# Optimization experiments

Hardware: AMD Instinct MI355X
Metric: run time of the kernel (lower is better)

Reference implementation:

```python
import jax, jax.numpy as jnp
import numpy as np

N_NODES = 50000
N_HYPEREDGES = 20000


def _segment_softmax(logits, seg, num_segments):
    mx = jax.ops.segment_max(logits, seg, num_segments=num_segments)
    mx = jnp.where(jnp.isfinite(mx), mx, 0.0)
    e = jnp.exp(logits - mx[seg])
    s = jax.ops.segment_sum(e, seg, num_segments=num_segments)
    return e / (s[seg] + 1e-16)


def _hypergraph_conv(x, he_node, he_edge, W, bias, num_nodes, num_he):
    # PyG HypergraphConv (use_attention=False, heads=1, hyperedge_weight=1):
    # out = D^{-1} H B^{-1} H^T (x W) + bias
    h = x @ W  # [N, C]
    ones = jnp.ones_like(he_node, dtype=h.dtype)
    D = jax.ops.segment_sum(ones, he_node, num_segments=num_nodes)
    Dinv = jnp.where(D > 0, 1.0 / D, 0.0)
    B = jax.ops.segment_sum(ones, he_edge, num_segments=num_he)
    Binv = jnp.where(B > 0, 1.0 / B, 0.0)
    # node -> hyperedge
    m = Binv[:, None] * jax.ops.segment_sum(h[he_node], he_edge, num_segments=num_he)
    # hyperedge -> node
    out = Dinv[:, None] * jax.ops.segment_sum(m[he_edge], he_node, num_segments=num_nodes)
    return out + bias


def _gat_conv(x, edge_index, W, a_src, a_dst, bias, num_nodes):
    # PyG GATConv defaults: heads=1, concat=True, slope=0.2, add_self_loops=True
    loops = jnp.arange(num_nodes)
    src = jnp.concatenate([edge_index[0], loops])
    dst = jnp.concatenate([edge_index[1], loops])
    h = x @ W  # [N, C]
    asrc = h @ a_src  # [N]
    adst = h @ a_dst  # [N]
    logit = jax.nn.leaky_relu(asrc[src] + adst[dst], negative_slope=0.2)
    alpha = _segment_softmax(logit, dst, num_nodes)  # softmax over incoming edges
    out = jax.ops.segment_sum(alpha[:, None] * h[src], dst, num_segments=num_nodes)
    return out + bias


def _mlp(e, Wm1, bm1, Wm2, bm2, Wm3, bm3, Wm4, bm4):
    # PyG MLP(128,64,3, num_layers=4) in eval mode: BN is identity at init,
    # dropout inactive -> Linear+ReLU chain, final Linear plain.
    h = jax.nn.relu(e @ Wm1 + bm1)
    h = jax.nn.relu(h @ Wm2 + bm2)
    h = jax.nn.relu(h @ Wm3 + bm3)
    return h @ Wm4 + bm4


def setup_inputs() -> dict:
    key = jax.random.key(0)
    ks = jax.random.split(key, 32)
    s = 0.05
    inp = {
        'x': jax.random.normal(ks[0], (N_NODES, 128), dtype=jnp.float32),
        'edge_index': jax.random.randint(ks[1], (2, 800000), 0, N_NODES),
        'he_node': jax.random.randint(ks[2], (400000,), 0, N_NODES),
        'he_edge': jax.random.randint(ks[3], (400000,), 0, N_HYPEREDGES),
        'edge_label_index': jax.random.randint(ks[4], (2, 100000), 0, N_NODES),
        'W1': jax.random.normal(ks[5], (128, 256)) * s,
        'b1': jnp.zeros((256,), jnp.float32),
        'W2': jax.random.normal(ks[6], (256, 256)) * s,
        'a2s': jax.random.normal(ks[7], (256,)) * s,
        'a2d': jax.random.normal(ks[8], (256,)) * s,
        'b2': jnp.zeros((256,), jnp.float32),
        'W3': jax.random.normal(ks[9], (256, 64)) * s,
        'a3s': jax.random.normal(ks[10], (64,)) * s,
        'a3d': jax.random.normal(ks[11], (64,)) * s,
        'b3': jnp.zeros((64,), jnp.float32),
        'Wm1': jax.random.normal(ks[12], (128, 64)) * s,
        'bm1': jnp.zeros((64,), jnp.float32),
        'Wm2': jax.random.normal(ks[13], (64, 64)) * s,
        'bm2': jnp.zeros((64,), jnp.float32),
        'Wm3': jax.random.normal(ks[14], (64, 64)) * s,
        'bm3': jnp.zeros((64,), jnp.float32),
        'Wm4': jax.random.normal(ks[15], (64, 3)) * s,
        'bm4': jnp.zeros((3,), jnp.float32),
    }
    return inp


def reference(x, edge_index, he_node, he_edge, edge_label_index,
              W1, b1, W2, a2s, a2d, b2, W3, a3s, a3d, b3,
              Wm1, bm1, Wm2, bm2, Wm3, bm3, Wm4, bm4):
    n = x.shape[0]
    # encode
    h = jax.nn.relu(_hypergraph_conv(x, he_node, he_edge, W1, b1, n, N_HYPEREDGES))
    h = jax.nn.relu(_gat_conv(h, edge_index, W2, a2s, a2d, b2, n))
    z = jax.nn.relu(_gat_conv(h, edge_index, W3, a3s, a3d, b3, n))
    # decode
    src, dst = edge_label_index[0], edge_label_index[1]
    edge_attr = jnp.concatenate([z[src], z[dst]], axis=-1)  # [L, 128]
    out = _mlp(edge_attr, Wm1, bm1, Wm2, bm2, Wm3, bm3, Wm4, bm4)  # [L, 3]
    out_pred = jnp.argmax(out, axis=-1)
    out_prob = jnp.take_along_axis(out, out_pred[:, None], axis=-1)[:, 0]
    return (out_pred, out_prob, out)
```

## Files before the change

kernel.cpp:

```cpp
#include <hip/hip_runtime.h>
#include <math.h>

#define NHE_CONST 20000

typedef float v4f __attribute__((ext_vector_type(4)));

__device__ __forceinline__ float lrelu(float x){ return x >= 0.f ? x : 0.2f * x; }

__global__ void k_count_all(const int* __restrict__ he_node, const int* __restrict__ he_edge, int inc,
                            const int* __restrict__ dst, int e,
                            int* cntN, int* cntHE, int* cntD){
  int i = blockIdx.x * blockDim.x + threadIdx.x;
  if (i < inc){ atomicAdd(&cntN[he_node[i]], 1); atomicAdd(&cntHE[he_edge[i]], 1); }
  if (i < e) atomicAdd(&cntD[dst[i]], 1);
}

__global__ __launch_bounds__(256) void k_scan_sums3(
    const int* __restrict__ p0, int n0, int* __restrict__ b0,
    const int* __restrict__ p1, int n1, int* __restrict__ b1,
    const int* __restrict__ p2, int n2, int* __restrict__ b2){
  const int* p; int n; int* bs;
  if (blockIdx.y == 0){ p = p0; n = n0; bs = b0; }
  else if (blockIdx.y == 1){ p = p1; n = n1; bs = b1; }
  else { p = p2; n = n2; bs = b2; }
  int nb = (n + 1023) / 1024;
  if ((int)blockIdx.x >= nb) return;
  __shared__ int sm[256];
  int base = blockIdx.x * 1024;
  int v = 0;
  for (int i = threadIdx.x; i < 1024; i += 256){
    int idx = base + i;
    v += (idx < n) ? p[idx] : 0;
  }
  sm[threadIdx.x] = v; __syncthreads();
  for (int d = 128; d > 0; d >>= 1){
    if (threadIdx.x < d) sm[threadIdx.x] += sm[threadIdx.x + d];
    __syncthreads();
  }
  if (threadIdx.x == 0) bs[blockIdx.x] = sm[0];
}

__global__ void k_scan_bsum3(int* b0, int nb0, int* b1, int nb1, int* b2, int nb2){
  int t = threadIdx.x;
  int* bs; int nb;
  if (t == 0){ bs = b0; nb = nb0; }
  else if (t == 1){ bs = b1; nb = nb1; }
  else if (t == 2){ bs = b2; nb = nb2; }
  else return;
  int acc = 0;
  for (int i = 0; i < nb; i++){ int v = bs[i]; bs[i] = acc; acc += v; }
}

__global__ __launch_bounds__(256) void k_scan_apply3(
    const int* __restrict__ c0, int n0, const int* __restrict__ s0, int* __restrict__ o0, int* __restrict__ u0,
    const int* __restrict__ c1, int n1, const int* __restrict__ s1, int* __restrict__ o1, int* __restrict__ u1,
    const int* __restrict__ c2, int n2, const int* __restrict__ s2, int* __restrict__ o2, int* __restrict__ u2){
  const int* cnt; int n; const int* bsum; int* off; int* cur;
  if (blockIdx.y == 0){ cnt = c0; n = n0; bsum = s0; off = o0; cur = u0; }
  else if (blockIdx.y == 1){ cnt = c1; n = n1; bsum = s1; off = o1; cur = u1; }
  else { cnt = c2; n = n2; bsum = s2; off = o2; cur = u2; }
  int nb = (n + 1023) / 1024;
  int b = blockIdx.x;
  if (b >= nb) return;
  __shared__ int sm[256];
  int base = b * 1024 + threadIdx.x * 4;
  int v[4];
  #pragma unroll
  for (int i = 0; i < 4; i++) v[i] = (base + i < n) ? cnt[base + i] : 0;
  int s = v[0] + v[1] + v[2] + v[3];
  sm[threadIdx.x] = s; __syncthreads();
  int x = s;
  for (int d = 1; d < 256; d <<= 1){
    int t = (threadIdx.x >= d) ? sm[threadIdx.x - d] : 0;
    __syncthreads();
    x += t; sm[threadIdx.x] = x;
    __syncthreads();
  }
  int run = x - s + bsum[b];
  #pragma unroll
  for (int i = 0; i < 4; i++){
    if (base + i < n) cur[base + i] = run;
    run += v[i];
    if (base + i < n) off[base + i + 1] = run;
  }
  if (b == 0 && threadIdx.x == 0) off[0] = 0;
}

__global__ __launch_bounds__(256) void k_fill_sliced(
    const int* __restrict__ he_node, const int* __restrict__ he_edge, int inc,
    const int* __restrict__ src, const int* __restrict__ dst, int e,
    int* curN, int* curHE, int* curD,
    int* __restrict__ nHEs, int* __restrict__ heNodes, int* __restrict__ srcIdx,
    int nN, int nHE){
  int slice = blockIdx.x & 7;
  int group = blockIdx.x >> 3;
  int ngroups = gridDim.x >> 3;
  int sN  = (nN  + 7) >> 3;  int loN  = slice * sN;  int hiN  = min(loN + sN, nN);
  int sHE = (nHE + 7) >> 3;  int loHE = slice * sHE; int hiHE = min(loHE + sHE, nHE);
  int stride = ngroups * 256;
  int start = group * 256 + threadIdx.x;
  for (int i = start; i < e; i += stride){
    int d = dst[i];
    if (d >= loN && d < hiN){
      int p = atomicAdd(&curD[d], 1);
      srcIdx[p] = src[i];
    }
  }
  for (int i = start; i < inc; i += stride){
    int nd = he_node[i], he = he_edge[i];
    if (nd >= loN && nd < hiN){
      int q = atomicAdd(&curN[nd], 1);
      nHEs[q] = he;
    }
    if (he >= loHE && he < hiHE){
      int p = atomicAdd(&curHE[he], 1);
      heNodes[p] = nd;
    }
  }
}

__global__ __launch_bounds__(256) void k_gemm_b64_bias(
    const float* __restrict__ A, const float* __restrict__ B, float* __restrict__ C,
    int M, int N, int K, const float* __restrict__ bias){
  __shared__ float As[16][132];
  __shared__ float Bs[16][64];
  int tid = threadIdx.x;
  int tn = tid & 15, tm = tid >> 4;
  int bm = blockIdx.x * 128, bn = blockIdx.y * 64;

  float acc[8][4];
  #pragma unroll
  for (int i = 0; i < 8; i++)
    #pragma unroll
    for (int j = 0; j < 4; j++) acc[i][j] = 0.f;

  int arow = tid >> 2, akc = (tid & 3) * 4;
  int brow = tid >> 4, bcol = (tid & 15) * 4;
  int gr0 = bm + arow, gr1 = gr0 + 64;

  float4 pa0, pa1, pb;
  pa0 = (gr0 < M) ? *(const float4*)(A + (size_t)gr0 * K + akc) : make_float4(0,0,0,0);
  pa1 = (gr1 < M) ? *(const float4*)(A + (size_t)gr1 * K + akc) : make_float4(0,0,0,0);
  pb  = *(const float4*)(B + (size_t)brow * N + bn + bcol);

  for (int k0 = 0; k0 < K; k0 += 16){
    As[akc + 0][arow] = pa0.x; As[akc + 1][arow] = pa0.y;
    As[akc + 2][arow] = pa0.z; As[akc + 3][arow] = pa0.w;
    As[akc + 0][arow + 64] = pa1.x; As[akc + 1][arow + 64] = pa1.y;
    As[akc + 2][arow + 64] = pa1.z; As[akc + 3][arow + 64] = pa1.w;
    *(float4*)&Bs[brow][bcol] = pb;
    __syncthreads();

    int k1 = k0 + 16;
    if (k1 < K){
      pa0 = (gr0 < M) ? *(const float4*)(A + (size_t)gr0 * K + k1 + akc) : make_float4(0,0,0,0);
      pa1 = (gr1 < M) ? *(const float4*)(A + (size_t)gr1 * K + k1 + akc) : make_float4(0,0,0,0);
      pb  = *(const float4*)(B + (size_t)(k1 + brow) * N + bn + bcol);
    }

    #pragma unroll
    for (int k = 0; k < 16; k++){
      float4 a0 = *(const float4*)&As[k][tm * 8];
      float4 a1 = *(const float4*)&As[k][tm * 8 + 4];
      float4 b  = *(const float4*)&Bs[k][tn * 4];
      float a[8] = {a0.x, a0.y, a0.z, a0.w, a1.x, a1.y, a1.z, a1.w};
      float bb[4] = {b.x, b.y, b.z, b.w};
      #pragma unroll
      for (int i = 0; i < 8; i++)
        #pragma unroll
        for (int j = 0; j < 4; j++) acc[i][j] += a[i] * bb[j];
    }
    __syncthreads();
  }
  float4 bv = *(const float4*)(bias + bn + tn * 4);
  #pragma unroll
  for (int i = 0; i < 8; i++){
    int r = bm + tm * 8 + i;
    if (r < M){
      *(float4*)(C + (size_t)r * N + bn + tn * 4) =
        make_float4(fmaxf(acc[i][0]+bv.x,0.f), fmaxf(acc[i][1]+bv.y,0.f),
                    fmaxf(acc[i][2]+bv.z,0.f), fmaxf(acc[i][3]+bv.w,0.f));
    }
  }
}

__global__ __launch_bounds__(256) void k_gemm_b64_dots(
    const float* __restrict__ A, const float* __restrict__ B, float* __restrict__ C,
    int M, int N, int K, const float* __restrict__ a_s, const float* __restrict__ a_d,
    float* __restrict__ vs, float* __restrict__ vd){
  __shared__ float As[16][132];
  __shared__ float Bs[16][64];
  int tid = threadIdx.x;
  int tn = tid & 15, tm = tid >> 4;
  int bm = blockIdx.x * 128, bn = blockIdx.y * 64;

  float acc[8][4];
  #pragma unroll
  for (int i = 0; i < 8; i++)
    #pragma unroll
    for (int j = 0; j < 4; j++) acc[i][j] = 0.f;

  int arow = tid >> 2, akc = (tid & 3) * 4;
  int brow = tid >> 4, bcol = (tid & 15) * 4;
  int gr0 = bm + arow, gr1 = gr0 + 64;

  float4 pa0, pa1, pb;
  pa0 = (gr0 < M) ? *(const float4*)(A + (size_t)gr0 * K + akc) : make_float4(0,0,0,0);
  pa1 = (gr1 < M) ? *(const float4*)(A + (size_t)gr1 * K + akc) : make_float4(0,0,0,0);
  pb  = *(const float4*)(B + (size_t)brow * N + bn + bcol);

  for (int k0 = 0; k0 < K; k0 += 16){
    As[akc + 0][arow] = pa0.x; As[akc + 1][arow] = pa0.y;
    As[akc + 2][arow] = pa0.z; As[akc + 3][arow] = pa0.w;
    As[akc + 0][arow + 64] = pa1.x; As[akc + 1][arow + 64] = pa1.y;
    As[akc + 2][arow + 64] = pa1.z; As[akc + 3][arow + 64] = pa1.w;
    *(float4*)&Bs[brow][bcol] = pb;
    __syncthreads();

    int k1 = k0 + 16;
    if (k1 < K){
      pa0 = (gr0 < M) ? *(const float4*)(A + (size_t)gr0 * K + k1 + akc) : make_float4(0,0,0,0);
      pa1 = (gr1 < M) ? *(const float4*)(A + (size_t)gr1 * K + k1 + akc) : make_float4(0,0,0,0);
      pb  = *(const float4*)(B + (size_t)(k1 + brow) * N + bn + bcol);
    }

    #pragma unroll
    for (int k = 0; k < 16; k++){
      float4 a0 = *(const float4*)&As[k][tm * 8];
      float4 a1 = *(const float4*)&As[k][tm * 8 + 4];
      float4 b  = *(const float4*)&Bs[k][tn * 4];
      float a[8] = {a0.x, a0.y, a0.z, a0.w, a1.x, a1.y, a1.z, a1.w};
      float bb[4] = {b.x, b.y, b.z, b.w};
      #pragma unroll
      for (int i = 0; i < 8; i++)
        #pragma unroll
        for (int j = 0; j < 4; j++) acc[i][j] += a[i] * bb[j];
    }
    __syncthreads();
  }
  float4 s = *(const float4*)(a_s + bn + tn * 4);
  float4 d = *(const float4*)(a_d + bn + tn * 4);
  #pragma unroll
  for (int i = 0; i < 8; i++){
    int r = bm + tm * 8 + i;
    if (r < M)
      *(float4*)(C + (size_t)r * N + bn + tn * 4) =
        make_float4(acc[i][0], acc[i][1], acc[i][2], acc[i][3]);
    float ps = acc[i][0]*s.x + acc[i][1]*s.y + acc[i][2]*s.z + acc[i][3]*s.w;
    float pd = acc[i][0]*d.x + acc[i][1]*d.y + acc[i][2]*d.z + acc[i][3]*d.w;
    ps += __shfl_xor(ps, 1); ps += __shfl_xor(ps, 2); ps += __shfl_xor(ps, 4); ps += __shfl_xor(ps, 8);
    pd += __shfl_xor(pd, 1); pd += __shfl_xor(pd, 2); pd += __shfl_xor(pd, 4); pd += __shfl_xor(pd, 8);
    if (tn == 0 && r < M){ atomicAdd(&vs[r], ps); atomicAdd(&vd[r], pd); }
  }
}

__global__ __launch_bounds__(256) void k_gemm64_dots(
    const float* __restrict__ A, const float* __restrict__ B, float* __restrict__ C,
    int M, int N, int K, const float* __restrict__ a_s, const float* __restrict__ a_d,
    float* __restrict__ vs, float* __restrict__ vd){
  __shared__ float As[16][68];
  __shared__ float Bs[16][64];
  int tid = threadIdx.x;
  int tn = tid & 15, tm = tid >> 4;
  int bm = blockIdx.x * 64;

  float acc[4][4];
  #pragma unroll
  for (int i = 0; i < 4; i++)
    #pragma unroll
    for (int j = 0; j < 4; j++) acc[i][j] = 0.f;

  int arow = tid >> 2, akc = (tid & 3) * 4;
  int brow = tid >> 4, bcol = (tid & 15) * 4;
  int gr = bm + arow;

  float4 pa, pb;
  pa = (gr < M) ? *(const float4*)(A + (size_t)gr * K + akc) : make_float4(0,0,0,0);
  pb = *(const float4*)(B + (size_t)brow * N + bcol);

  for (int k0 = 0; k0 < K; k0 += 16){
    As[akc + 0][arow] = pa.x; As[akc + 1][arow] = pa.y;
    As[akc + 2][arow] = pa.z; As[akc + 3][arow] = pa.w;
    *(float4*)&Bs[brow][bcol] = pb;
    __syncthreads();

    int k1 = k0 + 16;
    if (k1 < K){
      pa = (gr < M) ? *(const float4*)(A + (size_t)gr * K + k1 + akc) : make_float4(0,0,0,0);
      pb = *(const float4*)(B + (size_t)(k1 + brow) * N + bcol);
    }

    #pragma unroll
    for (int k = 0; k < 16; k++){
      float4 a = *(const float4*)&As[k][tm * 4];
      float4 b = *(const float4*)&Bs[k][tn * 4];
      float av[4] = {a.x, a.y, a.z, a.w};
      float bb[4] = {b.x, b.y, b.z, b.w};
      #pragma unroll
      for (int i = 0; i < 4; i++)
        #pragma unroll
        for (int j = 0; j < 4; j++) acc[i][j] += av[i] * bb[j];
    }
    __syncthreads();
  }
  float4 s = *(const float4*)(a_s + tn * 4);
  float4 d = *(const float4*)(a_d + tn * 4);
  #pragma unroll
  for (int i = 0; i < 4; i++){
    int r = bm + tm * 4 + i;
    if (r < M)
      *(float4*)(C + (size_t)r * N + tn * 4) = make_float4(acc[i][0], acc[i][1], acc[i][2], acc[i][3]);
    float ps = acc[i][0]*s.x + acc[i][1]*s.y + acc[i][2]*s.z + acc[i][3]*s.w;
    float pd = acc[i][0]*d.x + acc[i][1]*d.y + acc[i][2]*d.z + acc[i][3]*d.w;
    ps += __shfl_xor(ps, 1); ps += __shfl_xor(ps, 2); ps += __shfl_xor(ps, 4); ps += __shfl_xor(ps, 8);
    pd += __shfl_xor(pd, 1); pd += __shfl_xor(pd, 2); pd += __shfl_xor(pd, 4); pd += __shfl_xor(pd, 8);
    if (tn == 0 && r < M){ vs[r] = ps; vd[r] = pd; }
  }
}

__global__ __launch_bounds__(256) void k_hg_edge128(const float* __restrict__ x, const int* __restrict__ off,
                                                    const int* __restrict__ heNodes, float* __restrict__ mout,
                                                    int nhe){
  int wid = (blockIdx.x * blockDim.x + threadIdx.x) >> 6;
  int lane = threadIdx.x & 63;
  if (wid >= nhe) return;
  int s = off[wid], e = off[wid + 1];
  float2 a0 = make_float2(0,0), a1 = a0, a2 = a0, a3 = a0;
  int i = s;
  for (; i + 8 <= e; i += 8){
    int n8[8];
    #pragma unroll
    for (int u = 0; u < 8; u++) n8[u] = heNodes[i + u];
    float2 v8[8];
    #pragma unroll
    for (int u = 0; u < 8; u++) v8[u] = *(const float2*)(x + (size_t)n8[u] * 128 + lane * 2);
    #pragma unroll
    for (int u = 0; u < 8; u++){
      float2* c = (u & 3) == 0 ? &a0 : (u & 3) == 1 ? &a1 : (u & 3) == 2 ? &a2 : &a3;
      c->x += v8[u].x; c->y += v8[u].y;
    }
  }
  for (; i < e; i++){
    int nd = heNodes[i];
    float2 v = *(const float2*)(x + (size_t)nd * 128 + lane * 2);
    a0.x += v.x; a0.y += v.y;
  }
  float inv = (e > s) ? 1.f / (float)(e - s) : 0.f;
  float2 o = make_float2((a0.x + a1.x + a2.x + a3.x) * inv, (a0.y + a1.y + a2.y + a3.y) * inv);
  *(float2*)(mout + (size_t)wid * 128 + lane * 2) = o;
}

__global__ __launch_bounds__(256) void k_hg_node128(const float* __restrict__ m_in, const int* __restrict__ off,
                                                    const int* __restrict__ nHEs, float* __restrict__ out,
                                                    int nn){
  int wid = (blockIdx.x * blockDim.x + threadIdx.x) >> 6;
  int lane = threadIdx.x & 63;
  if (wid >= nn) return;
  int s = off[wid], e = off[wid + 1];
  float2 a0 = make_float2(0,0), a1 = a0, a2 = a0, a3 = a0;
  int i = s;
  for (; i + 4 <= e; i += 4){
    int n0 = nHEs[i], n1 = nHEs[i+1], n2 = nHEs[i+2], n3 = nHEs[i+3];
    float2 v0 = *(const float2*)(m_in + (size_t)n0 * 128 + lane * 2);
    float2 v1 = *(const float2*)(m_in + (size_t)n1 * 128 + lane * 2);
    float2 v2 = *(const float2*)(m_in + (size_t)n2 * 128 + lane * 2);
    float2 v3 = *(const float2*)(m_in + (size_t)n3 * 128 + lane * 2);
    a0.x += v0.x; a0.y += v0.y; a1.x += v1.x; a1.y += v1.y;
    a2.x += v2.x; a2.y += v2.y; a3.x += v3.x; a3.y += v3.y;
  }
  for (; i < e; i++){
    int he = nHEs[i];
    float2 v = *(const float2*)(m_in + (size_t)he * 128 + lane * 2);
    a0.x += v.x; a0.y += v.y;
  }
  float inv = (e > s) ? 1.f / (float)(e - s) : 0.f;
  float2 o = make_float2((a0.x + a1.x + a2.x + a3.x) * inv, (a0.y + a1.y + a2.y + a3.y) * inv);
  *(float2*)(out + (size_t)wid * 128 + lane * 2) = o;
}

__global__ __launch_bounds__(256) void k_gat256(const float* __restrict__ h, const float* __restrict__ asr,
                                                const float* __restrict__ ads, const int* __restrict__ off,
                                                const int* __restrict__ srcIdx, const float* __restrict__ bias,
                                                float* __restrict__ out, int nn){
  int wid = (blockIdx.x * blockDim.x + threadIdx.x) >> 6;
  int lane = threadIdx.x & 63;
  if (wid >= nn) return;
  float ad = ads[wid];
  int s = off[wid], e = off[wid + 1];

  float ssum = 0.f;
  float4 c0 = make_float4(0,0,0,0), c1 = c0, c2 = c0, c3 = c0;
  {
    float e0 = __expf(lrelu(asr[wid] + ad));
    ssum += e0;
    float4 v = *(const float4*)(h + (size_t)wid * 256 + lane * 4);
    c0.x += e0 * v.x; c0.y += e0 * v.y; c0.z += e0 * v.z; c0.w += e0 * v.w;
  }
  int i = s;
  for (; i + 8 <= e; i += 8){
    int n8[8];
    #pragma unroll
    for (int u = 0; u < 8; u++) n8[u] = srcIdx[i + u];
    float f8[8];
    #pragma unroll
    for (int u = 0; u < 8; u++) f8[u] = asr[n8[u]];
    float4 v8[8];
    #pragma unroll
    for (int u = 0; u < 8; u++) v8[u] = *(const float4*)(h + (size_t)n8[u] * 256 + lane * 4);
    #pragma unroll
    for (int u = 0; u < 8; u++){
      float ee = __expf(lrelu(f8[u] + ad));
      ssum += ee;
      float4* c = (u & 3) == 0 ? &c0 : (u & 3) == 1 ? &c1 : (u & 3) == 2 ? &c2 : &c3;
      c->x += ee * v8[u].x; c->y += ee * v8[u].y; c->z += ee * v8[u].z; c->w += ee * v8[u].w;
    }
  }
  for (; i < e; i++){
    int sn = srcIdx[i];
    float ee = __expf(lrelu(asr[sn] + ad));
    ssum += ee;
    float4 v = *(const float4*)(h + (size_t)sn * 256 + lane * 4);
    c0.x += ee * v.x; c0.y += ee * v.y; c0.z += ee * v.z; c0.w += ee * v.w;
  }
  float r = 1.f / (ssum + 1e-16f);
  float4 b = *(const float4*)(bias + lane * 4);
  v4f o;
  o.x = fmaxf((c0.x + c1.x + c2.x + c3.x) * r + b.x, 0.f);
  o.y = fmaxf((c0.y + c1.y + c2.y + c3.y) * r + b.y, 0.f);
  o.z = fmaxf((c0.z + c1.z + c2.z + c3.z) * r + b.z, 0.f);
  o.w = fmaxf((c0.w + c1.w + c2.w + c3.w) * r + b.w, 0.f);
  __builtin_nontemporal_store(o, (v4f*)(out + (size_t)wid * 256 + lane * 4));
}

__global__ __launch_bounds__(256) void k_gat64(const float* __restrict__ h, const float* __restrict__ asr,
                                               const float* __restrict__ ads, const int* __restrict__ off,
                                               const int* __restrict__ srcIdx, const float* __restrict__ bias,
                                               float* __restrict__ out, int nn){
  int wid = (blockIdx.x * blockDim.x + threadIdx.x) >> 6;
  int lane = threadIdx.x & 63;
  if (wid >= nn) return;
  float ad = ads[wid];
  int s = off[wid], e = off[wid + 1];

  float ssum = 0.f;
  float c0 = 0.f, c1 = 0.f, c2 = 0.f, c3 = 0.f;
  {
    float e0 = __expf(lrelu(asr[wid] + ad));
    ssum += e0;
    c0 += e0 * h[(size_t)wid * 64 + lane];
  }
  int i = s;
  for (; i + 8 <= e; i += 8){
    int n8[8];
    #pragma unroll
    for (int u = 0; u < 8; u++) n8[u] = srcIdx[i + u];
    float f8[8], v8[8];
    #pragma unroll
    for (int u = 0; u < 8; u++) f8[u] = asr[n8[u]];
    #pragma unroll
    for (int u = 0; u < 8; u++) v8[u] = h[(size_t)n8[u] * 64 + lane];
    #pragma unroll
    for (int u = 0; u < 8; u++){
      float ee = __expf(lrelu(f8[u] + ad));
      ssum += ee;
      if ((u & 3) == 0) c0 += ee * v8[u];
      else if ((u & 3) == 1) c1 += ee * v8[u];
      else if ((u & 3) == 2) c2 += ee * v8[u];
      else c3 += ee * v8[u];
    }
  }
  for (; i < e; i++){
    int sn = srcIdx[i];
    float ee = __expf(lrelu(asr[sn] + ad));
    ssum += ee;
    c0 += ee * h[(size_t)sn * 64 + lane];
  }
  float r = 1.f / (ssum + 1e-16f);
  out[(size_t)wid * 64 + lane] = fmaxf((c0 + c1 + c2 + c3) * r + bias[lane], 0.f);
}

#define DEC_EPB 128

__device__ __forceinline__ void dec_stageW(float (*Ws)[68], const float* __restrict__ W, int tid){
  #pragma unroll
  for (int i = 0; i < 4; i++){
    int idx = tid + i * 256;
    int r = idx >> 4, c = (idx & 15) * 4;
    *(float4*)&Ws[r][c] = *(const float4*)(W + r * 64 + c);
  }
}

__device__ __forceinline__ void dec_gather(float (*act)[132], const float* __restrict__ z,
                                           const int* __restrict__ idxv, int ebase, int wv, int lane, int L){
  #pragma unroll 4
  for (int t = 0; t < 32; t++){
    int le = wv * 32 + t;
    int e = ebase + le;
    int nd = (e < L) ? idxv[e] : 0;
    act[lane][le] = z[(size_t)nd * 64 + lane];
  }
}

__device__ __forceinline__ void dec_mac64(const float (*act)[132], const float (*Ws)[68],
                                          int tm, int tn, float (&acc)[8][4]){
  #pragma unroll 8
  for (int k = 0; k < 64; k++){
    float4 a0 = *(const float4*)&act[k][tm * 8];
    float4 a1 = *(const float4*)&act[k][tm * 8 + 4];
    float4 b  = *(const float4*)&Ws[k][tn * 4];
    float a[8] = {a0.x, a0.y, a0.z, a0.w, a1.x, a1.y, a1.z, a1.w};
    #pragma unroll
    for (int i = 0; i < 8; i++){
      acc[i][0] = fmaf(a[i], b.x, acc[i][0]);
      acc[i][1] = fmaf(a[i], b.y, acc[i][1]);
      acc[i][2] = fmaf(a[i], b.z, acc[i][2]);
      acc[i][3] = fmaf(a[i], b.w, acc[i][3]);
    }
  }
}

__device__ __forceinline__ void dec_writeback(float (*act)[132], int tm, int tn, const float (&acc)[8][4]){
  #pragma unroll
  for (int j = 0; j < 4; j++)
    #pragma unroll
    for (int i = 0; i < 8; i++)
      act[tn * 4 + j][tm * 8 + i] = fmaxf(acc[i][j], 0.f);
}

__global__ __launch_bounds__(256) void k_decode(const float* __restrict__ z, const int* __restrict__ eli, int L,
    const float* __restrict__ Wm1, const float* __restrict__ bm1,
    const float* __restrict__ Wm2, const float* __restrict__ bm2,
    const float* __restrict__ Wm3, const float* __restrict__ bm3,
    const float* __restrict__ Wm4, const float* __restrict__ bm4,
    float* __restrict__ outPred, float* __restrict__ outProb, float* __restrict__ outLog){
  __shared__ float act[64][132];
  __shared__ float Ws[64][68];
  __shared__ float W4s[192];
  __shared__ float b1s[64], b2s[64], b3s[64], b4s[4];

  int tid = threadIdx.x, lane = tid & 63, wv = tid >> 6;
  int tm = tid >> 4, tn = tid & 15;
  int ebase = blockIdx.x * DEC_EPB;

  if (tid < 64){ b1s[tid] = bm1[tid]; b2s[tid] = bm2[tid]; b3s[tid] = bm3[tid]; }
  if (tid < 3) b4s[tid] = bm4[tid];
  if (tid < 192) W4s[tid] = Wm4[tid];

  dec_stageW(Ws, Wm1, tid);
  dec_gather(act, z, eli, ebase, wv, lane, L);
  __syncthreads();

  float acc[8][4];
  {
    float bx = b1s[tn*4], by = b1s[tn*4+1], bz = b1s[tn*4+2], bw = b1s[tn*4+3];
    #pragma unroll
    for (int i = 0; i < 8; i++){ acc[i][0]=bx; acc[i][1]=by; acc[i][2]=bz; acc[i][3]=bw; }
  }
  dec_mac64(act, Ws, tm, tn, acc);
  __syncthreads();

  dec_stageW(Ws, Wm1 + 4096, tid);
  dec_gather(act, z, eli + L, ebase, wv, lane, L);
  __syncthreads();
  dec_mac64(act, Ws, tm, tn, acc);
  __syncthreads();

  dec_writeback(act, tm, tn, acc);
  dec_stageW(Ws, Wm2, tid);
  __syncthreads();

  {
    float bx = b2s[tn*4], by = b2s[tn*4+1], bz = b2s[tn*4+2], bw = b2s[tn*4+3];
    #pragma unroll
    for (int i = 0; i < 8; i++){ acc[i][0]=bx; acc[i][1]=by; acc[i][2]=bz; acc[i][3]=bw; }
  }
  dec_mac64(act, Ws, tm, tn, acc);
  __syncthreads();
  dec_writeback(act, tm, tn, acc);
  dec_stageW(Ws, Wm3, tid);
  __syncthreads();

  {
    float bx = b3s[tn*4], by = b3s[tn*4+1], bz = b3s[tn*4+2], bw = b3s[tn*4+3];
    #pragma unroll
    for (int i = 0; i < 8; i++){ acc[i][0]=bx; acc[i][1]=by; acc[i][2]=bz; acc[i][3]=bw; }
  }
  dec_mac64(act, Ws, tm, tn, acc);
  __syncthreads();
  dec_writeback(act, tm, tn, acc);
  __syncthreads();

  if (tid < DEC_EPB){
    int e = tid;
    float o0 = b4s[0], o1 = b4s[1], o2 = b4s[2];
    #pragma unroll 8
    for (int k = 0; k < 64; k++){
      float av = act[k][e];
      o0 = fmaf(av, W4s[k*3+0], o0);
      o1 = fmaf(av, W4s[k*3+1], o1);
      o2 = fmaf(av, W4s[k*3+2], o2);
    }
    int eg = ebase + e;
    if (eg < L){
      int am = 0; float best = o0;
      if (o1 > best){ am = 1; best = o1; }
      if (o2 > best){ am = 2; best = o2; }
      outPred[eg] = (float)am;
      outProb[eg] = best;
      outLog[(size_t)eg * 3 + 0] = o0;
      outLog[(size_t)eg * 3 + 1] = o1;
      outLog[(size_t)eg * 3 + 2] = o2;
    }
  }
}

extern "C" void kernel_launch(void* const* d_in, const int* in_sizes, int n_in,
                              void* d_out, int out_size, void* d_ws, size_t ws_size,
                              hipStream_t stream){
  const float* x      = (const float*)d_in[0];
  const int*   ei     = (const int*)d_in[1];
  const int*   he_node= (const int*)d_in[2];
  const int*   he_edge= (const int*)d_in[3];
  const int*   eli    = (const int*)d_in[4];
  const float* W1  = (const float*)d_in[5];
  const float* b1  = (const float*)d_in[6];
  const float* W2  = (const float*)d_in[7];
  const float* a2s = (const float*)d_in[8];
  const float* a2d = (const float*)d_in[9];
  const float* b2  = (const float*)d_in[10];
  const float* W3  = (const float*)d_in[11];
  const float* a3s = (const float*)d_in[12];
  const float* a3d = (const float*)d_in[13];
  const float* b3  = (const float*)d_in[14];
  const float* Wm1 = (const float*)d_in[15]; const float* bm1 = (const float*)d_in[16];
  const float* Wm2 = (const float*)d_in[17]; const float* bm2 = (const float*)d_in[18];
  const float* Wm3 = (const float*)d_in[19]; const float* bm3 = (const float*)d_in[20];
  const float* Wm4 = (const float*)d_in[21]; const float* bm4 = (const float*)d_in[22];

  const int N   = in_sizes[0] / 128;
  const int E   = in_sizes[1] / 2;
  const int INC = in_sizes[2];
  const int NHE = NHE_CONST;
  const int L   = in_sizes[4] / 2;

  char* wbase = (char*)d_ws;
  size_t woff = 0;
  auto walloc = [&](size_t bytes) -> void* {
    void* p = wbase + woff;
    woff = (woff + bytes + 255) & ~(size_t)255;
    return p;
  };
  float* pre1   = (float*)walloc((size_t)N * 128 * 4);
  float* mbuf   = (float*)walloc((size_t)NHE * 128 * 4);
  float* h1     = (float*)walloc((size_t)N * 256 * 4);
  float* t2     = (float*)walloc((size_t)N * 256 * 4);
  float* t3     = (float*)walloc((size_t)N * 64 * 4);
  float* zbuf   = (float*)walloc((size_t)N * 64 * 4);
  float* vboth  = (float*)walloc((size_t)2 * N * 4);
  int* heOff  = (int*)walloc((size_t)(NHE + 1) * 4);
  int* nOff   = (int*)walloc((size_t)(N + 1) * 4);
  int* dOff   = (int*)walloc((size_t)(N + 1) * 4);
  int* cntAll = (int*)walloc((size_t)(NHE + 2 * N) * 4);
  int* curAll = (int*)walloc((size_t)(NHE + 2 * N) * 4);
  int* heNodes= (int*)walloc((size_t)INC * 4);
  int* nHEs   = (int*)walloc((size_t)INC * 4);
  int* srcIdx = (int*)walloc((size_t)E * 4);
  int* bsumA  = (int*)walloc(64 * 4);
  int* bsumB  = (int*)walloc(64 * 4);
  int* bsumC  = (int*)walloc(64 * 4);

  int* cntHE = cntAll;           int* cntN = cntAll + NHE; int* cntD = cntAll + NHE + N;
  int* curHE = curAll;           int* curN = curAll + NHE; int* curD = curAll + NHE + N;
  float* vsrc = vboth;           float* vdst = vboth + N;
  float* h2 = h1;

  const int* srcPtr = ei;
  const int* dstPtr = ei + E;

  hipMemsetAsync(cntAll, 0, (size_t)(NHE + 2 * N) * 4, stream);
  hipMemsetAsync(vboth,  0, (size_t)2 * N * 4, stream);
  k_count_all<<<(E + 255) / 256, 256, 0, stream>>>(he_node, he_edge, INC, dstPtr, E, cntN, cntHE, cntD);

  int nbHE = (NHE + 1023) / 1024;
  int nbN  = (N + 1023) / 1024;
  k_scan_sums3<<<dim3(nbN, 3), 256, 0, stream>>>(cntHE, NHE, bsumA, cntN, N, bsumB, cntD, N, bsumC);
  k_scan_bsum3<<<1, 64, 0, stream>>>(bsumA, nbHE, bsumB, nbN, bsumC, nbN);
  k_scan_apply3<<<dim3(nbN, 3), 256, 0, stream>>>(cntHE, NHE, bsumA, heOff, curHE,
                                                  cntN,  N,   bsumB, nOff,  curN,
                                                  cntD,  N,   bsumC, dOff,  curD);
  k_fill_sliced<<<8 * 128, 256, 0, stream>>>(he_node, he_edge, INC, srcPtr, dstPtr, E,
                                             curN, curHE, curD, nHEs, heNodes, srcIdx, N, NHE);

  int gRowA = (N + 127) / 128;
  int gRowB = (N + 63) / 64;
  int gWav  = (N + 3) / 4;

  k_hg_edge128<<<(NHE + 3) / 4, 256, 0, stream>>>(x, heOff, heNodes, mbuf, NHE);
  k_hg_node128<<<gWav, 256, 0, stream>>>(mbuf, nOff, nHEs, pre1, N);
  k_gemm_b64_bias<<<dim3(gRowA, 4), 256, 0, stream>>>(pre1, W1, h1, N, 256, 128, b1);

  k_gemm_b64_dots<<<dim3(gRowA, 4), 256, 0, stream>>>(h1, W2, t2, N, 256, 256, a2s, a2d, vsrc, vdst);
  k_gat256<<<gWav, 256, 0, stream>>>(t2, vsrc, vdst, dOff, srcIdx, b2, h2, N);

  k_gemm64_dots<<<gRowB, 256, 0, stream>>>(h2, W3, t3, N, 64, 256, a3s, a3d, vsrc, vdst);
  k_gat64<<<gWav, 256, 0, stream>>>(t3, vsrc, vdst, dOff, srcIdx, b3, zbuf, N);

  float* outPred = (float*)d_out;
  float* outProb = outPred + L;
  float* outLog  = outProb + L;
  k_decode<<<(L + DEC_EPB - 1) / DEC_EPB, 256, 0, stream>>>(zbuf, eli, L,
                                    Wm1, bm1, Wm2, bm2, Wm3, bm3, Wm4, bm4,
                                    outPred, outProb, outLog);
}
```

Baseline: 798.1 us.

## Halve decoder edges per block and prefetch second gather into registers

The edge decoder MLP block now handles 64 edges instead of 128, so each thread computes a 4x4 register tile instead of 8x4 and the shared activation buffer shrinks. The dst-side z gather is issued into registers together with the src-side gather, before the first matmul, then written to shared memory after it. This hides gather latency and doubles the grid for better occupancy, at the cost of more blocks re-staging the same weights and less reuse of each weight load from shared memory.

```diff
diff --git a/kernel.cpp b/kernel.cpp
--- a/kernel.cpp
+++ b/kernel.cpp
@@ -479,7 +479,7 @@
   out[(size_t)wid * 64 + lane] = fmaxf((c0 + c1 + c2 + c3) * r + bias[lane], 0.f);
 }
 
-#define DEC_EPB 128
+#define DEC_EPB 64
 
 __device__ __forceinline__ void dec_stageW(float (*Ws)[68], const float* __restrict__ W, int tid){
   #pragma unroll
@@ -490,41 +490,28 @@
   }
 }
 
-__device__ __forceinline__ void dec_gather(float (*act)[132], const float* __restrict__ z,
-                                           const int* __restrict__ idxv, int ebase, int wv, int lane, int L){
-  #pragma unroll 4
-  for (int t = 0; t < 32; t++){
-    int le = wv * 32 + t;
-    int e = ebase + le;
-    int nd = (e < L) ? idxv[e] : 0;
-    act[lane][le] = z[(size_t)nd * 64 + lane];
-  }
-}
-
-__device__ __forceinline__ void dec_mac64(const float (*act)[132], const float (*Ws)[68],
-                                          int tm, int tn, float (&acc)[8][4]){
+__device__ __forceinline__ void dec_mac4(const float (*act)[68], const float (*Ws)[68],
+                                         int tm, int tn, float (&acc)[4][4]){
   #pragma unroll 8
   for (int k = 0; k < 64; k++){
-    float4 a0 = *(const float4*)&act[k][tm * 8];
-    float4 a1 = *(const float4*)&act[k][tm * 8 + 4];
-    float4 b  = *(const float4*)&Ws[k][tn * 4];
-    float a[8] = {a0.x, a0.y, a0.z, a0.w, a1.x, a1.y, a1.z, a1.w};
-    #pragma unroll
-    for (int i = 0; i < 8; i++){
-      acc[i][0] = fmaf(a[i], b.x, acc[i][0]);
-      acc[i][1] = fmaf(a[i], b.y, acc[i][1]);
-      acc[i][2] = fmaf(a[i], b.z, acc[i][2]);
-      acc[i][3] = fmaf(a[i], b.w, acc[i][3]);
-    }
-  }
-}
-
-__device__ __forceinline__ void dec_writeback(float (*act)[132], int tm, int tn, const float (&acc)[8][4]){
+    float4 a = *(const float4*)&act[k][tm * 4];
+    float4 b = *(const float4*)&Ws[k][tn * 4];
+    float av[4] = {a.x, a.y, a.z, a.w};
+    float bb[4] = {b.x, b.y, b.z, b.w};
+    #pragma unroll
+    for (int i = 0; i < 4; i++)
+      #pragma unroll
+      for (int j = 0; j < 4; j++)
+        acc[i][j] = fmaf(av[i], bb[j], acc[i][j]);
+  }
+}
+
+__device__ __forceinline__ void dec_writeback4(float (*act)[68], int tm, int tn, const float (&acc)[4][4]){
   #pragma unroll
   for (int j = 0; j < 4; j++)
     #pragma unroll
-    for (int i = 0; i < 8; i++)
-      act[tn * 4 + j][tm * 8 + i] = fmaxf(acc[i][j], 0.f);
+    for (int i = 0; i < 4; i++)
+      act[tn * 4 + j][tm * 4 + i] = fmaxf(acc[i][j], 0.f);
 }
 
 __global__ __launch_bounds__(256) void k_decode(const float* __restrict__ z, const int* __restrict__ eli, int L,
@@ -533,7 +520,7 @@
     const float* __restrict__ Wm3, const float* __restrict__ bm3,
     const float* __restrict__ Wm4, const float* __restrict__ bm4,
     float* __restrict__ outPred, float* __restrict__ outProb, float* __restrict__ outLog){
-  __shared__ float act[64][132];
+  __shared__ float act[64][68];
   __shared__ float Ws[64][68];
   __shared__ float W4s[192];
   __shared__ float b1s[64], b2s[64], b3s[64], b4s[4];
@@ -547,47 +534,61 @@
   if (tid < 192) W4s[tid] = Wm4[tid];
 
   dec_stageW(Ws, Wm1, tid);
-  dec_gather(act, z, eli, ebase, wv, lane, L);
-  __syncthreads();
-
-  float acc[8][4];
+  #pragma unroll
+  for (int t = 0; t < 16; t++){
+    int le = wv * 16 + t;
+    int e = ebase + le;
+    int nd = (e < L) ? eli[e] : 0;
+    act[lane][le] = z[(size_t)nd * 64 + lane];
+  }
+  float g[16];
+  #pragma unroll
+  for (int t = 0; t < 16; t++){
+    int e = ebase + wv * 16 + t;
+    int nd = (e < L) ? eli[L + e] : 0;
+    g[t] = z[(size_t)nd * 64 + lane];
+  }
+  __syncthreads();
+
+  float acc[4][4];
   {
     float bx = b1s[tn*4], by = b1s[tn*4+1], bz = b1s[tn*4+2], bw = b1s[tn*4+3];
     #pragma unroll
-    for (int i = 0; i < 8; i++){ acc[i][0]=bx; acc[i][1]=by; acc[i][2]=bz; acc[i][3]=bw; }
-  }
-  dec_mac64(act, Ws, tm, tn, acc);
-  __syncthreads();
-
+    for (int i = 0; i < 4; i++){ acc[i][0]=bx; acc[i][1]=by; acc[i][2]=bz; acc[i][3]=bw; }
+  }
+  dec_mac4(act, Ws, tm, tn, acc);
+  __syncthreads();
+
+  #pragma unroll
+  for (int t = 0; t < 16; t++) act[lane][wv * 16 + t] = g[t];
   dec_stageW(Ws, Wm1 + 4096, tid);
-  dec_gather(act, z, eli + L, ebase, wv, lane, L);
-  __syncthreads();
-  dec_mac64(act, Ws, tm, tn, acc);
-  __syncthreads();
-
-  dec_writeback(act, tm, tn, acc);
+  __syncthreads();
+  dec_mac4(act, Ws, tm, tn, acc);
+  __syncthreads();
+
+  dec_writeback4(act, tm, tn, acc);
   dec_stageW(Ws, Wm2, tid);
   __syncthreads();
 
   {
     float bx = b2s[tn*4], by = b2s[tn*4+1], bz = b2s[tn*4+2], bw = b2s[tn*4+3];
     #pragma unroll
-    for (int i = 0; i < 8; i++){ acc[i][0]=bx; acc[i][1]=by; acc[i][2]=bz; acc[i][3]=bw; }
-  }
-  dec_mac64(act, Ws, tm, tn, acc);
-  __syncthreads();
-  dec_writeback(act, tm, tn, acc);
+    for (int i = 0; i < 4; i++){ acc[i][0]=bx; acc[i][1]=by; acc[i][2]=bz; acc[i][3]=bw; }
+  }
+  dec_mac4(act, Ws, tm, tn, acc);
+  __syncthreads();
+  dec_writeback4(act, tm, tn, acc);
   dec_stageW(Ws, Wm3, tid);
   __syncthreads();
 
   {
     float bx = b3s[tn*4], by = b3s[tn*4+1], bz = b3s[tn*4+2], bw = b3s[tn*4+3];
     #pragma unroll
-    for (int i = 0; i < 8; i++){ acc[i][0]=bx; acc[i][1]=by; acc[i][2]=bz; acc[i][3]=bw; }
-  }
-  dec_mac64(act, Ws, tm, tn, acc);
-  __syncthreads();
-  dec_writeback(act, tm, tn, acc);
+    for (int i = 0; i < 4; i++){ acc[i][0]=bx; acc[i][1]=by; acc[i][2]=bz; acc[i][3]=bw; }
+  }
+  dec_mac4(act, Ws, tm, tn, acc);
+  __syncthreads();
+  dec_writeback4(act, tm, tn, acc);
   __syncthreads();
 
   if (tid < DEC_EPB){
```

Result: faster. 724.7 us (-9.2%).
